# Optimization experiments

Measured on AMD Instinct MI355X. Metric: run time of the kernel, lower is better.

## Reference

```python
import jax, jax.numpy as jnp
import numpy as np

N_NODES = 100000
N_EDGES = 1600000
IN_DIM, HID_DIM, OUT_DIM = 128, 128, 1


def gcn_conv(x, W, b, src, dst, n_nodes):
    """PyG-style GCNConv: add self-loops, symmetric D^-1/2 (A+I) D^-1/2 normalization.

    x: [N, F_in], W: [F_in, F_out], b: [F_out], src/dst: [E] int edge endpoints.
    """
    h = x @ W  # [N, F_out] transform first (as PyG does)
    # degree on A + I, counted over destination (symmetric graph assumption)
    ones = jnp.ones(src.shape[0], dtype=h.dtype)
    deg = jax.ops.segment_sum(ones, dst, num_segments=n_nodes) + 1.0  # +1 self loop
    dinv = jax.lax.rsqrt(deg)  # [N]
    norm = dinv[src] * dinv[dst]  # [E] edge normalization
    msg = h[src] * norm[:, None]  # [E, F_out] gather + scale
    agg = jax.ops.segment_sum(msg, dst, num_segments=n_nodes)  # scatter-add
    # self-loop contribution: norm_ii = dinv[i]^2
    out = agg + h * (dinv * dinv)[:, None]
    return out + b


def setup_inputs() -> dict:
    key = jax.random.key(0)
    k1, k2, k3, k4 = jax.random.split(key, 4)
    x = jax.random.normal(k1, (N_NODES, IN_DIM), dtype=jnp.float32)
    edge_index = jax.random.randint(k2, (2, N_EDGES), 0, N_NODES, dtype=jnp.int64)
    W1 = jax.random.normal(k3, (IN_DIM, HID_DIM), dtype=jnp.float32) * (1.0 / np.sqrt(IN_DIM))
    b1 = jnp.zeros((HID_DIM,), dtype=jnp.float32)
    W2 = jax.random.normal(k4, (HID_DIM, OUT_DIM), dtype=jnp.float32) * (1.0 / np.sqrt(HID_DIM))
    b2 = jnp.zeros((OUT_DIM,), dtype=jnp.float32)
    return {"x": x, "edge_index": edge_index, "W1": W1, "b1": b1, "W2": W2, "b2": b2}


def reference(x, edge_index, W1, b1, W2, b2):
    n = x.shape[0]
    src, dst = edge_index[0], edge_index[1]
    h = gcn_conv(x, W1, b1, src, dst, n)
    h = jax.nn.relu(h)
    # dropout(p=0.2) is identity at inference
    out = gcn_conv(h, W2, b2, src, dst, n)  # [N, 1]
    return out
```

## Files before the change

kernel.cpp:

```cpp
#include <hip/hip_runtime.h>

#define N_NODES 100000
#define N_EDGES 1600000
#define DIM 128

#define BSHIFT 8
#define BNODES 256
#define NBUCK 391
#define BCAP  4608
#define PCHUNK 4096
#define NB_PART ((N_EDGES + PCHUNK - 1) / PCHUNK)

#define GTILES 1563
#define GSTRIDE 391

#define HALF_ELEMS ((size_t)N_NODES * 64)

typedef short s16x8 __attribute__((ext_vector_type(8)));
typedef float f32x4 __attribute__((ext_vector_type(4)));

__device__ __forceinline__ unsigned short f2bf(float f) {
    unsigned u = __float_as_uint(f);
    u += 0x7fffu + ((u >> 16) & 1u);
    return (unsigned short)(u >> 16);
}
__device__ __forceinline__ float bflo(unsigned u) { return __uint_as_float(u << 16); }
__device__ __forceinline__ float bfhi(unsigned u) { return __uint_as_float(u & 0xffff0000u); }

__device__ __forceinline__ void acc8(float (&a)[8], uint4 v, float w) {
    a[0] = fmaf(bflo(v.x), w, a[0]); a[1] = fmaf(bfhi(v.x), w, a[1]);
    a[2] = fmaf(bflo(v.y), w, a[2]); a[3] = fmaf(bfhi(v.y), w, a[3]);
    a[4] = fmaf(bflo(v.z), w, a[4]); a[5] = fmaf(bfhi(v.z), w, a[5]);
    a[6] = fmaf(bflo(v.w), w, a[6]); a[7] = fmaf(bfhi(v.w), w, a[7]);
}


__global__ void k_zero(int* __restrict__ gcur) {
    int t = blockIdx.x * blockDim.x + threadIdx.x;
    if (t < NBUCK) gcur[t] = t * BCAP;
}

__device__ __forceinline__ void part_body(char* smem, int bid,
                                          const int* __restrict__ src,
                                          const int* __restrict__ dst,
                                          int* __restrict__ gcur,
                                          int2* __restrict__ ebuf) {
    int* hist = (int*)smem;
    int* gbase = hist + NBUCK;
    int tid = threadIdx.x;
    long e0 = (long)bid * PCHUNK;
    int n = min(PCHUNK, (int)(N_EDGES - e0));
    for (int b = tid; b < NBUCK; b += 256) hist[b] = 0;
    __syncthreads();

    int mys[16], myd[16];
#pragma unroll
    for (int k = 0; k < 16; ++k) {
        int idx = k * 256 + tid;
        if (idx < n) {
            mys[k] = src[e0 + idx];
            myd[k] = dst[e0 + idx];
            atomicAdd(&hist[myd[k] >> BSHIFT], 1);
        } else {
            myd[k] = -1;
        }
    }
    __syncthreads();
    for (int b = tid; b < NBUCK; b += 256) {
        gbase[b] = hist[b] ? atomicAdd(&gcur[b], hist[b]) : 0;
        hist[b] = 0;
    }
    __syncthreads();
#pragma unroll
    for (int k = 0; k < 16; ++k) {
        if (myd[k] >= 0) {
            int b = myd[k] >> BSHIFT;
            int slot = gbase[b] + atomicAdd(&hist[b], 1);
            ebuf[slot] = make_int2(mys[k], myd[k]);
        }
    }
}

__device__ __forceinline__ void csr_body(char* smem, int b,
                                         const int2* __restrict__ ebuf,
                                         const int* __restrict__ gcur,
                                         int* __restrict__ rp,
                                         int* __restrict__ cnt,
                                         float* __restrict__ dinv,
                                         int* __restrict__ csrs) {
    int* lcnt = (int*)smem;
    int* lcur = lcnt + BNODES;
    int t = threadIdx.x;
    int node0 = b << BSHIFT;
    lcnt[t] = 0;
    __syncthreads();
    int base = b * BCAP, end = gcur[b];
    for (int e = base + t; e < end; e += 256)
        atomicAdd(&lcnt[ebuf[e].y - node0], 1);
    __syncthreads();
    int c = lcnt[t];
    lcur[t] = c;
    __syncthreads();
    for (int s = 1; s < 256; s <<= 1) {
        int u = (t >= s) ? lcur[t - s] : 0;
        __syncthreads();
        lcur[t] += u;
        __syncthreads();
    }
    int excl = lcur[t] - c;
    lcur[t] = excl;
    int node = node0 + t;
    if (node < N_NODES) {
        rp[node] = base + excl;
        cnt[node] = c;
        dinv[node] = rsqrtf((float)(c + 1));
    }
    __syncthreads();
    for (int e = base + t; e < end; e += 256) {
        int2 d = ebuf[e];
        int p = atomicAdd(&lcur[d.y - node0], 1);
        csrs[base + p] = d.x;
    }
}

__device__ __forceinline__ void gemm_body(char* smem, int bid,
                                          const float* __restrict__ x,
                                          const float* __restrict__ W1,
                                          unsigned short* __restrict__ h1h) {
    unsigned short* Wt = (unsigned short*)smem;
    int tid = threadIdx.x;
    for (int idx = tid; idx < DIM * DIM; idx += 256) {
        int k = idx >> 7, c = idx & 127;
        Wt[c * 128 + (k ^ ((c & 7) << 3))] = f2bf(W1[idx]);
    }
    __syncthreads();

    int wv = tid >> 6, lane = tid & 63;
    int g = lane >> 4, tl = lane & 15;
    unsigned short* cst = (unsigned short*)(smem + 32768 + wv * 4096);
    int hf = tl >> 3, ch = (tl & 7) * 8;

    for (int tile = bid; tile < GTILES; tile += GSTRIDE) {
        int rb = tile * 64 + wv * 16;
        if (rb >= N_NODES) continue;

        s16x8 afrag[4];
        const float* xrow = x + (size_t)(rb + tl) * DIM + g * 8;
#pragma unroll
        for (int kc = 0; kc < 4; ++kc) {
            float4 p0 = *(const float4*)(xrow + kc * 32);
            float4 p1 = *(const float4*)(xrow + kc * 32 + 4);
            s16x8 a;
            a[0] = (short)f2bf(p0.x); a[1] = (short)f2bf(p0.y);
            a[2] = (short)f2bf(p0.z); a[3] = (short)f2bf(p0.w);
            a[4] = (short)f2bf(p1.x); a[5] = (short)f2bf(p1.y);
            a[6] = (short)f2bf(p1.z); a[7] = (short)f2bf(p1.w);
            afrag[kc] = a;
        }

        f32x4 acc[8];
#pragma unroll
        for (int ct = 0; ct < 8; ++ct) acc[ct] = (f32x4)0.0f;
#pragma unroll
        for (int kc = 0; kc < 4; ++kc) {
#pragma unroll
            for (int ct = 0; ct < 8; ++ct) {
                int crow = ct * 16 + tl;
                int boff = crow * 256 + ((kc * 64 + g * 16) ^ ((crow & 7) << 4));
                s16x8 b = *(const s16x8*)((const char*)Wt + boff);
                acc[ct] = __builtin_amdgcn_mfma_f32_16x16x32_bf16(afrag[kc], b, acc[ct], 0, 0, 0);
            }
        }

#pragma unroll
        for (int ct = 0; ct < 8; ++ct) {
#pragma unroll
            for (int r = 0; r < 4; ++r) {
                float own = acc[ct][r];
                float oth = __shfl_xor(own, 1, 64);
                if ((lane & 1) == 0) {
                    unsigned pk = (unsigned)f2bf(own) | ((unsigned)f2bf(oth) << 16);
                    int row = g * 4 + r;
                    int col = ct * 16 + tl;
                    *(unsigned*)&cst[row * 128 + (col ^ (row << 3))] = pk;
                }
            }
        }
        asm volatile("s_waitcnt lgkmcnt(0)" ::: "memory");

#pragma unroll
        for (int c = 0; c < 4; ++c) {
            int row = c * 4 + g;
            uint4 v = *(const uint4*)&cst[row * 128 + ((tl ^ row) * 8)];
            *(uint4*)(h1h + (size_t)hf * HALF_ELEMS + (size_t)(rb + row) * 64 + ch) = v;
        }
        __syncthreads();
    }
}

__global__ __launch_bounds__(256) void k_part(const int* __restrict__ src,
                                              const int* __restrict__ dst,
                                              int* __restrict__ gcur,
                                              int2* __restrict__ ebuf) {
    __shared__ __align__(16) char smem[2 * NBUCK * 4 + 16];
    part_body(smem, blockIdx.x, src, dst, gcur, ebuf);
}

__global__ __launch_bounds__(256) void k_gemm(const float* __restrict__ x,
                                              const float* __restrict__ W1,
                                              unsigned short* __restrict__ h1h) {
    __shared__ __align__(16) char smem[49152];
    gemm_body(smem, blockIdx.x, x, W1, h1h);
}

__global__ __launch_bounds__(256) void k_csrk(const int2* __restrict__ ebuf,
                                              const int* __restrict__ gcur,
                                              int* __restrict__ rp,
                                              int* __restrict__ cnt,
                                              float* __restrict__ dinv,
                                              int* __restrict__ csrs) {
    __shared__ __align__(16) char smem[2 * BNODES * 4];
    csr_body(smem, blockIdx.x, ebuf, gcur, rp, cnt, dinv, csrs);
}

__global__ __launch_bounds__(256) void k_pg(const int* __restrict__ src,
                                            const int* __restrict__ dst,
                                            int* __restrict__ gcur,
                                            int2* __restrict__ ebuf,
                                            const float* __restrict__ x,
                                            const float* __restrict__ W1,
                                            unsigned short* __restrict__ h1h) {
    __shared__ __align__(16) char smem[49152];
    if (blockIdx.x < NB_PART) part_body(smem, blockIdx.x, src, dst, gcur, ebuf);
    else                      gemm_body(smem, blockIdx.x - NB_PART, x, W1, h1h);
}


__global__ __launch_bounds__(256) void k_agg1h(const unsigned short* __restrict__ h1h,
                                               const float* __restrict__ dinv,
                                               const int* __restrict__ rp,
                                               const int* __restrict__ cnt,
                                               const int* __restrict__ csrs,
                                               const float* __restrict__ b1,
                                               const float* __restrict__ W2,
                                               float* __restrict__ zpart) {
    int half = blockIdx.x & 1;
    int nb = blockIdx.x >> 1;
    int lane = threadIdx.x & 63;
    int wv = threadIdx.x >> 6;
    int g = lane >> 3, tl = lane & 7;
    int i = nb * 32 + wv * 8 + g;
    int c0 = tl * 8;
    const unsigned short* hbase = h1h + (size_t)half * HALF_ELEMS + c0;
    float di = dinv[i];
    int beg = rp[i], end = beg + cnt[i];
    float a[8];
#pragma unroll
    for (int q = 0; q < 8; ++q) a[q] = 0.f;

    int j = beg;
    for (; j + 4 <= end; j += 4) {
        int s0 = csrs[j], s1 = csrs[j + 1], s2 = csrs[j + 2], s3 = csrs[j + 3];
        uint4 v0 = *(const uint4*)(hbase + (size_t)s0 * 64);
        uint4 v1 = *(const uint4*)(hbase + (size_t)s1 * 64);
        uint4 v2 = *(const uint4*)(hbase + (size_t)s2 * 64);
        uint4 v3 = *(const uint4*)(hbase + (size_t)s3 * 64);
        float w0 = dinv[s0] * di, w1 = dinv[s1] * di;
        float w2 = dinv[s2] * di, w3 = dinv[s3] * di;
        acc8(a, v0, w0);
        acc8(a, v1, w1);
        acc8(a, v2, w2);
        acc8(a, v3, w3);
    }
    for (; j < end; ++j) {
        int s0 = csrs[j];
        uint4 v0 = *(const uint4*)(hbase + (size_t)s0 * 64);
        acc8(a, v0, dinv[s0] * di);
    }

    uint4 vs = *(const uint4*)(hbase + (size_t)i * 64);
    float sii = di * di;
    int cb = half * 64 + c0;
    float4 bA = *(const float4*)(b1 + cb);
    float4 bB = *(const float4*)(b1 + cb + 4);
    float4 wA = *(const float4*)(W2 + cb);
    float4 wB = *(const float4*)(W2 + cb + 4);
    float p = 0.f;
    p += fmaxf(fmaf(bflo(vs.x), sii, a[0]) + bA.x, 0.f) * wA.x;
    p += fmaxf(fmaf(bfhi(vs.x), sii, a[1]) + bA.y, 0.f) * wA.y;
    p += fmaxf(fmaf(bflo(vs.y), sii, a[2]) + bA.z, 0.f) * wA.z;
    p += fmaxf(fmaf(bfhi(vs.y), sii, a[3]) + bA.w, 0.f) * wA.w;
    p += fmaxf(fmaf(bflo(vs.z), sii, a[4]) + bB.x, 0.f) * wB.x;
    p += fmaxf(fmaf(bfhi(vs.z), sii, a[5]) + bB.y, 0.f) * wB.y;
    p += fmaxf(fmaf(bflo(vs.w), sii, a[6]) + bB.z, 0.f) * wB.z;
    p += fmaxf(fmaf(bfhi(vs.w), sii, a[7]) + bB.w, 0.f) * wB.w;
#pragma unroll
    for (int off = 4; off >= 1; off >>= 1) p += __shfl_xor(p, off, 64);
    if (tl == 0) zpart[(size_t)half * N_NODES + i] = p;
}

__global__ void k_zred(const float* __restrict__ zpart, float* __restrict__ z) {
    int i = blockIdx.x * blockDim.x + threadIdx.x;
    if (i < N_NODES) z[i] = zpart[i] + zpart[N_NODES + i];
}


__global__ __launch_bounds__(256) void k_agg2(const float* __restrict__ zin,
                                              const float* __restrict__ dinv,
                                              const int* __restrict__ rp,
                                              const int* __restrict__ cnt,
                                              const int* __restrict__ csrs,
                                              const float* __restrict__ b2,
                                              float* __restrict__ out) {
    int i = blockIdx.x * blockDim.x + threadIdx.x;
    if (i >= N_NODES) return;
    float di = dinv[i];
    int beg = rp[i], end = beg + cnt[i];
    float acc = 0.f;
    int j = beg;
    for (; j + 4 <= end; j += 4) {
        int s0 = csrs[j], s1 = csrs[j + 1], s2 = csrs[j + 2], s3 = csrs[j + 3];
        float z0 = zin[s0], z1 = zin[s1], z2 = zin[s2], z3 = zin[s3];
        acc = fmaf(z0, dinv[s0] * di, acc);
        acc = fmaf(z1, dinv[s1] * di, acc);
        acc = fmaf(z2, dinv[s2] * di, acc);
        acc = fmaf(z3, dinv[s3] * di, acc);
    }
    for (; j < end; ++j) {
        int s0 = csrs[j];
        acc = fmaf(zin[s0], dinv[s0] * di, acc);
    }
    out[i] = acc + zin[i] * di * di + b2[0];
}


extern "C" void kernel_launch(void* const* d_in, const int* in_sizes, int n_in,
                              void* d_out, int out_size, void* d_ws, size_t ws_size,
                              hipStream_t stream) {
    const float* x  = (const float*)d_in[0];
    const int*   ei = (const int*)d_in[1];
    const float* W1 = (const float*)d_in[2];
    const float* b1 = (const float*)d_in[3];
    const float* W2 = (const float*)d_in[4];
    const float* b2 = (const float*)d_in[5];
    float* out = (float*)d_out;

    const int* src = ei;
    const int* dst = ei + N_EDGES;

    char* ws = (char*)d_ws;
    size_t o = 0;
    auto take = [&](size_t bytes) { char* p = ws + o; o += (bytes + 255) & ~(size_t)255; return p; };
    int*   cnt   = (int*)take(sizeof(int) * N_NODES);
    int*   rp    = (int*)take(sizeof(int) * N_NODES);
    int*   gcur  = (int*)take(sizeof(int) * (NBUCK + 1));
    float* dinv  = (float*)take(sizeof(float) * N_NODES);
    float* z     = (float*)take(sizeof(float) * N_NODES);
    float* zpart = (float*)take(sizeof(float) * 2 * N_NODES);
    int*   csrs  = (int*)take(sizeof(int) * (size_t)NBUCK * BCAP);
    unsigned short* h1h = (unsigned short*)take(sizeof(unsigned short) * 2 * HALF_ELEMS);
    int2* ebuf_sep = (int2*)take(sizeof(int2) * (size_t)NBUCK * BCAP);
    bool fused = (o <= ws_size);
    int2* ebuf = fused ? ebuf_sep : (int2*)h1h;

    const int NB_N = (N_NODES + 255) / 256;

    k_zero<<<2, 256, 0, stream>>>(gcur);
    if (fused) {
        k_pg<<<NB_PART + GSTRIDE, 256, 0, stream>>>(src, dst, gcur, ebuf, x, W1, h1h);
        k_csrk<<<NBUCK, 256, 0, stream>>>(ebuf, gcur, rp, cnt, dinv, csrs);
    } else {
        k_part<<<NB_PART, 256, 0, stream>>>(src, dst, gcur, ebuf);
        k_csrk<<<NBUCK, 256, 0, stream>>>(ebuf, gcur, rp, cnt, dinv, csrs);
        k_gemm<<<GSTRIDE, 256, 0, stream>>>(x, W1, h1h);
    }
    k_agg1h<<<2 * (N_NODES / 32), 256, 0, stream>>>(h1h, dinv, rp, cnt, csrs, b1, W2, zpart);
    k_zred<<<NB_N, 256, 0, stream>>>(zpart, z);
    k_agg2<<<NB_N, 256, 0, stream>>>(z, dinv, rp, cnt, csrs, b2, out);
}
```

Measured before the change: 144.5 us.

## Pack edge buffer into 32-bit, one GEMM tile per block, fold zred into agg2

Edges in the bucket buffer are packed as (src<<8 | local dst) in a single int instead of an int2. This halves the scatter and re-read traffic in partition and CSR construction. The GEMM drops its grid-stride loop and launches one block per 64-row tile, so every block re-converts W1 into shared memory. The separate zpart reduction kernel is folded into agg2, which now uses four threads per node with shuffle reduction; this removes one launch but does the zpart sum on every gather, and the packing relies on src fitting in 24 bits.

```diff
diff --git a/kernel.cpp b/kernel.cpp
--- a/kernel.cpp
+++ b/kernel.cpp
@@ -12,7 +12,6 @@
 #define NB_PART ((N_EDGES + PCHUNK - 1) / PCHUNK)
 
 #define GTILES 1563
-#define GSTRIDE 391
 
 #define HALF_ELEMS ((size_t)N_NODES * 64)
 
@@ -44,7 +43,7 @@
                                           const int* __restrict__ src,
                                           const int* __restrict__ dst,
                                           int* __restrict__ gcur,
-                                          int2* __restrict__ ebuf) {
+                                          int* __restrict__ ebuf) {
     int* hist = (int*)smem;
     int* gbase = hist + NBUCK;
     int tid = threadIdx.x;
@@ -53,16 +52,17 @@
     for (int b = tid; b < NBUCK; b += 256) hist[b] = 0;
     __syncthreads();
 
-    int mys[16], myd[16];
+    int pk[16], mybk[16];
 #pragma unroll
     for (int k = 0; k < 16; ++k) {
         int idx = k * 256 + tid;
         if (idx < n) {
-            mys[k] = src[e0 + idx];
-            myd[k] = dst[e0 + idx];
-            atomicAdd(&hist[myd[k] >> BSHIFT], 1);
+            int s = src[e0 + idx], d = dst[e0 + idx];
+            mybk[k] = d >> BSHIFT;
+            pk[k] = (s << 8) | (d & 255);
+            atomicAdd(&hist[mybk[k]], 1);
         } else {
-            myd[k] = -1;
+            mybk[k] = -1;
         }
     }
     __syncthreads();
@@ -73,16 +73,16 @@
     __syncthreads();
 #pragma unroll
     for (int k = 0; k < 16; ++k) {
-        if (myd[k] >= 0) {
-            int b = myd[k] >> BSHIFT;
+        if (mybk[k] >= 0) {
+            int b = mybk[k];
             int slot = gbase[b] + atomicAdd(&hist[b], 1);
-            ebuf[slot] = make_int2(mys[k], myd[k]);
+            ebuf[slot] = pk[k];
         }
     }
 }
 
 __device__ __forceinline__ void csr_body(char* smem, int b,
-                                         const int2* __restrict__ ebuf,
+                                         const int* __restrict__ ebuf,
                                          const int* __restrict__ gcur,
                                          int* __restrict__ rp,
                                          int* __restrict__ cnt,
@@ -96,7 +96,7 @@
     __syncthreads();
     int base = b * BCAP, end = gcur[b];
     for (int e = base + t; e < end; e += 256)
-        atomicAdd(&lcnt[ebuf[e].y - node0], 1);
+        atomicAdd(&lcnt[ebuf[e] & 255], 1);
     __syncthreads();
     int c = lcnt[t];
     lcur[t] = c;
@@ -117,16 +117,17 @@
     }
     __syncthreads();
     for (int e = base + t; e < end; e += 256) {
-        int2 d = ebuf[e];
-        int p = atomicAdd(&lcur[d.y - node0], 1);
-        csrs[base + p] = d.x;
-    }
-}
-
-__device__ __forceinline__ void gemm_body(char* smem, int bid,
+        int pkd = ebuf[e];
+        int p = atomicAdd(&lcur[pkd & 255], 1);
+        csrs[base + p] = (int)((unsigned)pkd >> 8);
+    }
+}
+
+__device__ __forceinline__ void gemm_body(char* smem, int tile,
                                           const float* __restrict__ x,
                                           const float* __restrict__ W1,
                                           unsigned short* __restrict__ h1h) {
+    if (tile >= GTILES) return;
     unsigned short* Wt = (unsigned short*)smem;
     int tid = threadIdx.x;
     for (int idx = tid; idx < DIM * DIM; idx += 256) {
@@ -138,70 +139,67 @@
     int wv = tid >> 6, lane = tid & 63;
     int g = lane >> 4, tl = lane & 15;
     unsigned short* cst = (unsigned short*)(smem + 32768 + wv * 4096);
-    int hf = tl >> 3, ch = (tl & 7) * 8;
-
-    for (int tile = bid; tile < GTILES; tile += GSTRIDE) {
-        int rb = tile * 64 + wv * 16;
-        if (rb >= N_NODES) continue;
-
-        s16x8 afrag[4];
-        const float* xrow = x + (size_t)(rb + tl) * DIM + g * 8;
-#pragma unroll
-        for (int kc = 0; kc < 4; ++kc) {
-            float4 p0 = *(const float4*)(xrow + kc * 32);
-            float4 p1 = *(const float4*)(xrow + kc * 32 + 4);
-            s16x8 a;
-            a[0] = (short)f2bf(p0.x); a[1] = (short)f2bf(p0.y);
-            a[2] = (short)f2bf(p0.z); a[3] = (short)f2bf(p0.w);
-            a[4] = (short)f2bf(p1.x); a[5] = (short)f2bf(p1.y);
-            a[6] = (short)f2bf(p1.z); a[7] = (short)f2bf(p1.w);
-            afrag[kc] = a;
+
+    int rb = tile * 64 + wv * 16;
+    if (rb >= N_NODES) return;
+
+    s16x8 afrag[4];
+    const float* xrow = x + (size_t)(rb + tl) * DIM + g * 8;
+#pragma unroll
+    for (int kc = 0; kc < 4; ++kc) {
+        float4 p0 = *(const float4*)(xrow + kc * 32);
+        float4 p1 = *(const float4*)(xrow + kc * 32 + 4);
+        s16x8 a;
+        a[0] = (short)f2bf(p0.x); a[1] = (short)f2bf(p0.y);
+        a[2] = (short)f2bf(p0.z); a[3] = (short)f2bf(p0.w);
+        a[4] = (short)f2bf(p1.x); a[5] = (short)f2bf(p1.y);
+        a[6] = (short)f2bf(p1.z); a[7] = (short)f2bf(p1.w);
+        afrag[kc] = a;
+    }
+
+    f32x4 acc[8];
+#pragma unroll
+    for (int ct = 0; ct < 8; ++ct) acc[ct] = (f32x4)0.0f;
+#pragma unroll
+    for (int kc = 0; kc < 4; ++kc) {
+#pragma unroll
+        for (int ct = 0; ct < 8; ++ct) {
+            int crow = ct * 16 + tl;
+            int boff = crow * 256 + ((kc * 64 + g * 16) ^ ((crow & 7) << 4));
+            s16x8 b = *(const s16x8*)((const char*)Wt + boff);
+            acc[ct] = __builtin_amdgcn_mfma_f32_16x16x32_bf16(afrag[kc], b, acc[ct], 0, 0, 0);
         }
-
-        f32x4 acc[8];
-#pragma unroll
-        for (int ct = 0; ct < 8; ++ct) acc[ct] = (f32x4)0.0f;
-#pragma unroll
-        for (int kc = 0; kc < 4; ++kc) {
-#pragma unroll
-            for (int ct = 0; ct < 8; ++ct) {
-                int crow = ct * 16 + tl;
-                int boff = crow * 256 + ((kc * 64 + g * 16) ^ ((crow & 7) << 4));
-                s16x8 b = *(const s16x8*)((const char*)Wt + boff);
-                acc[ct] = __builtin_amdgcn_mfma_f32_16x16x32_bf16(afrag[kc], b, acc[ct], 0, 0, 0);
+    }
+
+#pragma unroll
+    for (int ct = 0; ct < 8; ++ct) {
+#pragma unroll
+        for (int r = 0; r < 4; ++r) {
+            float own = acc[ct][r];
+            float oth = __shfl_xor(own, 1, 64);
+            if ((lane & 1) == 0) {
+                unsigned pk = (unsigned)f2bf(own) | ((unsigned)f2bf(oth) << 16);
+                int row = g * 4 + r;
+                int col = ct * 16 + tl;
+                *(unsigned*)&cst[row * 128 + (col ^ (row << 3))] = pk;
             }
         }
-
-#pragma unroll
-        for (int ct = 0; ct < 8; ++ct) {
-#pragma unroll
-            for (int r = 0; r < 4; ++r) {
-                float own = acc[ct][r];
-                float oth = __shfl_xor(own, 1, 64);
-                if ((lane & 1) == 0) {
-                    unsigned pk = (unsigned)f2bf(own) | ((unsigned)f2bf(oth) << 16);
-                    int row = g * 4 + r;
-                    int col = ct * 16 + tl;
-                    *(unsigned*)&cst[row * 128 + (col ^ (row << 3))] = pk;
-                }
-            }
-        }
-        asm volatile("s_waitcnt lgkmcnt(0)" ::: "memory");
-
-#pragma unroll
-        for (int c = 0; c < 4; ++c) {
-            int row = c * 4 + g;
-            uint4 v = *(const uint4*)&cst[row * 128 + ((tl ^ row) * 8)];
-            *(uint4*)(h1h + (size_t)hf * HALF_ELEMS + (size_t)(rb + row) * 64 + ch) = v;
-        }
-        __syncthreads();
+    }
+    asm volatile("s_waitcnt lgkmcnt(0)" ::: "memory");
+
+    int hf = tl >> 3, ch = (tl & 7) * 8;
+#pragma unroll
+    for (int c = 0; c < 4; ++c) {
+        int row = c * 4 + g;
+        uint4 v = *(const uint4*)&cst[row * 128 + ((tl ^ row) * 8)];
+        *(uint4*)(h1h + (size_t)hf * HALF_ELEMS + (size_t)(rb + row) * 64 + ch) = v;
     }
 }
 
 __global__ __launch_bounds__(256) void k_part(const int* __restrict__ src,
                                               const int* __restrict__ dst,
                                               int* __restrict__ gcur,
-                                              int2* __restrict__ ebuf) {
+                                              int* __restrict__ ebuf) {
     __shared__ __align__(16) char smem[2 * NBUCK * 4 + 16];
     part_body(smem, blockIdx.x, src, dst, gcur, ebuf);
 }
@@ -213,7 +211,7 @@
     gemm_body(smem, blockIdx.x, x, W1, h1h);
 }
 
-__global__ __launch_bounds__(256) void k_csrk(const int2* __restrict__ ebuf,
+__global__ __launch_bounds__(256) void k_csrk(const int* __restrict__ ebuf,
                                               const int* __restrict__ gcur,
                                               int* __restrict__ rp,
                                               int* __restrict__ cnt,
@@ -226,7 +224,7 @@
 __global__ __launch_bounds__(256) void k_pg(const int* __restrict__ src,
                                             const int* __restrict__ dst,
                                             int* __restrict__ gcur,
-                                            int2* __restrict__ ebuf,
+                                            int* __restrict__ ebuf,
                                             const float* __restrict__ x,
                                             const float* __restrict__ W1,
                                             unsigned short* __restrict__ h1h) {
@@ -299,38 +297,31 @@
     if (tl == 0) zpart[(size_t)half * N_NODES + i] = p;
 }
 
-__global__ void k_zred(const float* __restrict__ zpart, float* __restrict__ z) {
-    int i = blockIdx.x * blockDim.x + threadIdx.x;
-    if (i < N_NODES) z[i] = zpart[i] + zpart[N_NODES + i];
-}
-
-
-__global__ __launch_bounds__(256) void k_agg2(const float* __restrict__ zin,
+
+__global__ __launch_bounds__(256) void k_agg2(const float* __restrict__ zpart,
                                               const float* __restrict__ dinv,
                                               const int* __restrict__ rp,
                                               const int* __restrict__ cnt,
                                               const int* __restrict__ csrs,
                                               const float* __restrict__ b2,
                                               float* __restrict__ out) {
-    int i = blockIdx.x * blockDim.x + threadIdx.x;
+    int grp = threadIdx.x >> 2, r = threadIdx.x & 3;
+    int i = blockIdx.x * 64 + grp;
     if (i >= N_NODES) return;
     float di = dinv[i];
     int beg = rp[i], end = beg + cnt[i];
     float acc = 0.f;
-    int j = beg;
-    for (; j + 4 <= end; j += 4) {
-        int s0 = csrs[j], s1 = csrs[j + 1], s2 = csrs[j + 2], s3 = csrs[j + 3];
-        float z0 = zin[s0], z1 = zin[s1], z2 = zin[s2], z3 = zin[s3];
-        acc = fmaf(z0, dinv[s0] * di, acc);
-        acc = fmaf(z1, dinv[s1] * di, acc);
-        acc = fmaf(z2, dinv[s2] * di, acc);
-        acc = fmaf(z3, dinv[s3] * di, acc);
-    }
-    for (; j < end; ++j) {
-        int s0 = csrs[j];
-        acc = fmaf(zin[s0], dinv[s0] * di, acc);
-    }
-    out[i] = acc + zin[i] * di * di + b2[0];
+    for (int j = beg + r; j < end; j += 4) {
+        int s = csrs[j];
+        float zs = zpart[s] + zpart[N_NODES + s];
+        acc = fmaf(zs, dinv[s] * di, acc);
+    }
+    acc += __shfl_xor(acc, 1, 64);
+    acc += __shfl_xor(acc, 2, 64);
+    if (r == 0) {
+        float zi = zpart[i] + zpart[N_NODES + i];
+        out[i] = acc + zi * di * di + b2[0];
+    }
 }
 
 
@@ -355,26 +346,22 @@
     int*   rp    = (int*)take(sizeof(int) * N_NODES);
     int*   gcur  = (int*)take(sizeof(int) * (NBUCK + 1));
     float* dinv  = (float*)take(sizeof(float) * N_NODES);
-    float* z     = (float*)take(sizeof(float) * N_NODES);
     float* zpart = (float*)take(sizeof(float) * 2 * N_NODES);
     int*   csrs  = (int*)take(sizeof(int) * (size_t)NBUCK * BCAP);
     unsigned short* h1h = (unsigned short*)take(sizeof(unsigned short) * 2 * HALF_ELEMS);
-    int2* ebuf_sep = (int2*)take(sizeof(int2) * (size_t)NBUCK * BCAP);
+    int* ebuf_sep = (int*)take(sizeof(int) * (size_t)NBUCK * BCAP);
     bool fused = (o <= ws_size);
-    int2* ebuf = fused ? ebuf_sep : (int2*)h1h;
-
-    const int NB_N = (N_NODES + 255) / 256;
+    int* ebuf = fused ? ebuf_sep : (int*)h1h;
 
     k_zero<<<2, 256, 0, stream>>>(gcur);
     if (fused) {
-        k_pg<<<NB_PART + GSTRIDE, 256, 0, stream>>>(src, dst, gcur, ebuf, x, W1, h1h);
+        k_pg<<<NB_PART + GTILES, 256, 0, stream>>>(src, dst, gcur, ebuf, x, W1, h1h);
         k_csrk<<<NBUCK, 256, 0, stream>>>(ebuf, gcur, rp, cnt, dinv, csrs);
     } else {
         k_part<<<NB_PART, 256, 0, stream>>>(src, dst, gcur, ebuf);
         k_csrk<<<NBUCK, 256, 0, stream>>>(ebuf, gcur, rp, cnt, dinv, csrs);
-        k_gemm<<<GSTRIDE, 256, 0, stream>>>(x, W1, h1h);
+        k_gemm<<<GTILES, 256, 0, stream>>>(x, W1, h1h);
     }
     k_agg1h<<<2 * (N_NODES / 32), 256, 0, stream>>>(h1h, dinv, rp, cnt, csrs, b1, W2, zpart);
-    k_zred<<<NB_N, 256, 0, stream>>>(zpart, z);
-    k_agg2<<<NB_N, 256, 0, stream>>>(z, dinv, rp, cnt, csrs, b2, out);
-}
+    k_agg2<<<(N_NODES + 63) / 64, 256, 0, stream>>>(zpart, dinv, rp, cnt, csrs, b2, out);
+}
```

Result: no change. 143.9 us (-0.4%).
